# Performance work log

Measured on AMD Instinct MI355X. Metric: run time of the kernel, lower is better.

The kernel has to match this reference:

```python
import jax, jax.numpy as jnp
import numpy as np

N = 50000
E = 800000
F_IN = 2      # num_node_features
H = 2         # heads
C = 64        # embedding_size (per-head out channels)
HID = 128     # hidden_size (message dim)
B = 512       # number of messages
NEG_SLOPE = 0.2


def gatv2_conv(x, src, dst, edge_attr, Wl, bl, Wr, br, We, att, bias):
    # x: [N, F_IN]; src/dst: [E]; edge_attr: [E, 1]
    n = x.shape[0]
    xl = (x @ Wl + bl).reshape(n, H, C)   # source transform (lin_l)
    xr = (x @ Wr + br).reshape(n, H, C)   # target transform (lin_r)
    ea = (edge_attr @ We).reshape(-1, H, C)
    m = xl[src] + xr[dst] + ea                      # [E, H, C]
    e = jnp.where(m > 0, m, NEG_SLOPE * m)          # LeakyReLU
    score = jnp.einsum('ehc,hc->eh', e, att)        # [E, H]
    # scatter-softmax over incoming edges of each target node
    smax = jax.ops.segment_max(score, dst, num_segments=n)
    smax = jnp.where(jnp.isfinite(smax), smax, 0.0)
    ex = jnp.exp(score - smax[dst])
    denom = jax.ops.segment_sum(ex, dst, num_segments=n)
    alpha = ex / (denom[dst] + 1e-16)               # [E, H]
    out = jax.ops.segment_sum(xl[src] * alpha[:, :, None], dst, num_segments=n)
    return out.reshape(n, H * C) + bias


def setup_inputs() -> dict:
    key = jax.random.key(0)
    ks = jax.random.split(key, 20)
    s = 0.1
    inp = {
        'message': jax.random.normal(ks[0], (B, HID), jnp.float32),
        'x': jax.random.normal(ks[1], (N, F_IN), jnp.float32),
        'edge_index': jax.random.randint(ks[2], (2, E), 0, N, jnp.int32),
        'edge_attr': jax.random.normal(ks[3], (E, 1), jnp.float32),
    }
    def conv_params(base):
        return {
            'Wl': jax.random.normal(ks[base], (F_IN, H * C)) * s,
            'bl': jnp.zeros((H * C,), jnp.float32),
            'Wr': jax.random.normal(ks[base + 1], (F_IN, H * C)) * s,
            'br': jnp.zeros((H * C,), jnp.float32),
            'We': jax.random.normal(ks[base + 2], (1, H * C)) * s,
            'att': jax.random.normal(ks[base + 3], (H, C)) * s,
            'bias': jnp.zeros((H * C,), jnp.float32),
        }
    p1 = {k + '1': v for k, v in conv_params(4).items()}
    p2 = {k + '2': v for k, v in conv_params(8).items()}
    inp.update(p1)
    inp.update(p2)
    inp['Wfc'] = jax.random.normal(ks[12], (HID, H * C)) * s
    inp['bfc'] = jnp.zeros((H * C,), jnp.float32)
    return inp


def reference(message, x, edge_index, edge_attr,
              Wl1, bl1, Wr1, br1, We1, att1, bias1,
              Wl2, bl2, Wr2, br2, We2, att2, bias2,
              Wfc, bfc):
    src, dst = edge_index[0], edge_index[1]
    # conv1 output is computed but unused in the original forward (conv2 takes x again)
    h1 = jax.nn.relu(gatv2_conv(x, src, dst, edge_attr, Wl1, bl1, Wr1, br1, We1, att1, bias1))
    h = jax.nn.relu(gatv2_conv(x, src, dst, edge_attr, Wl2, bl2, Wr2, br2, We2, att2, bias2))
    msg = jnp.concatenate([message, message], axis=0)      # [2B, HID]
    msg_emb = msg @ Wfc + bfc                              # [2B, H*C]
    dot = h @ msg_emb.T                                    # [N, 2B]
    return jax.nn.softmax(dot, axis=0)
```

## Files before the change

kernel.cpp:

```cpp
#include <hip/hip_runtime.h>
#include <hip/hip_bf16.h>
#include <hip/hip_cooperative_groups.h>

namespace cg = cooperative_groups;

#define N_NODES 50000
#define N_PAD   50048
#define N_EDGES 800000
#define GRID    512
#define BLK     256
#define STRIDE  (GRID*BLK)
#define CHUNK   98
#define NTILES  782
#define NB_SCAN 196

typedef __attribute__((ext_vector_type(8))) short short8;
typedef __attribute__((ext_vector_type(16))) float f32x16;

struct Params {
  const float* msg; const float* x; const int* ei; const float* ea;
  const float* Wl; const float* bl; const float* Wr; const float* br;
  const float* We; const float* att; const float* bias;
  const float* Wfc; const float* bfc;
  float4* rec; float* nodeF;
  __hip_bfloat16* me_hi; __hip_bfloat16* me_lo;
  int* cnt; float* colsum; int* offs; int* cursor; int* bsum;
  float* dout;
};

template<int PASS>
__device__ __forceinline__ void mfma_tile(const Params& P, int tile, char* SMEM)
{
  short8* Bt = (short8*)SMEM;
  float* colacc = (float*)(SMEM + 32768);
  float* xp     = (float*)(SMEM + 32768);
  float* rcol   = (float*)(SMEM + 50176);

  const int tid = threadIdx.x;
  const int l = tid & 63, w = tid >> 6;
  const int rt = w >> 1, ct = w & 1;
  const int lrow = l & 31, lhalf = l >> 5;
  const int m0 = tile * 64;
  const int row = m0 + rt * 32 + lrow;

  float c0a = 0.f, c0b = 0.f, c0d = 0.f, c1a = 0.f, c1b = 0.f, c1d = 0.f;
  bool live = row < N_NODES;
  if (live) {
    const float* nf = P.nodeF + (size_t)row * 8;
    float D0 = nf[0], A00 = nf[1], A10 = nf[2];
    float D1 = nf[3], A01 = nf[4], A11 = nf[5];
    float r0 = 1.0f / (D0 + 1e-16f), r1 = 1.0f / (D1 + 1e-16f);
    c0a = A00 * r0; c0b = A10 * r0; c0d = D0 * r0;
    c1a = A01 * r1; c1b = A11 * r1; c1d = D1 * r1;
  }
  short8 a_hi[8], a_lo[8];
  #pragma unroll
  for (int ks = 0; ks < 8; ++ks) {
    int k0 = ks * 16 + lhalf * 8;
    float ca = (ks < 4) ? c0a : c1a;
    float cbv = (ks < 4) ? c0b : c1b;
    float cd = (ks < 4) ? c0d : c1d;
    float wA[8], wB[8], wC[8], wD[8];
    *(float4*)&wA[0] = *(const float4*)(P.Wl + k0);
    *(float4*)&wA[4] = *(const float4*)(P.Wl + k0 + 4);
    *(float4*)&wB[0] = *(const float4*)(P.Wl + 128 + k0);
    *(float4*)&wB[4] = *(const float4*)(P.Wl + 128 + k0 + 4);
    *(float4*)&wC[0] = *(const float4*)(P.bl + k0);
    *(float4*)&wC[4] = *(const float4*)(P.bl + k0 + 4);
    *(float4*)&wD[0] = *(const float4*)(P.bias + k0);
    *(float4*)&wD[4] = *(const float4*)(P.bias + k0 + 4);
    short8 hi8, lo8;
    #pragma unroll
    for (int j = 0; j < 8; ++j) {
      float v = ca * wA[j] + cbv * wB[j] + cd * wC[j] + wD[j];
      v = (live && v > 0.f) ? v : 0.f;
      __hip_bfloat16 hb = __float2bfloat16(v);
      float rem = v - __bfloat162float(hb);
      __hip_bfloat16 lb = __float2bfloat16(rem);
      short hs, ls;
      __builtin_memcpy(&hs, &hb, 2);
      __builtin_memcpy(&ls, &lb, 2);
      hi8[j] = hs; lo8[j] = ls;
    }
    a_hi[ks] = hi8; a_lo[ks] = lo8;
  }

  for (int cb = 0; cb < 8; ++cb) {
    __syncthreads();
    #pragma unroll
    for (int q = 0; q < 4; ++q) {
      int lin = q * 256 + tid;
      int col = lin >> 4, ku = lin & 15;
      int slot = col * 16 + (ku ^ (col & 7));
      size_t gb = ((size_t)(cb * 64 + col) << 7) + ku * 8;
      Bt[slot] = *(const short8*)(P.me_hi + gb);
      Bt[1024 + slot] = *(const short8*)(P.me_lo + gb);
    }
    __syncthreads();

    f32x16 acc = {0.f};
    #pragma unroll
    for (int ks = 0; ks < 8; ++ks) {
      int ku = ks * 2 + lhalf;
      int colB = ct * 32 + lrow;
      int slot = colB * 16 + (ku ^ (colB & 7));
      short8 bh = Bt[slot];
      short8 blo = Bt[1024 + slot];
      acc = __builtin_amdgcn_mfma_f32_32x32x16_bf16(a_hi[ks], bh, acc, 0, 0, 0);
      acc = __builtin_amdgcn_mfma_f32_32x32x16_bf16(a_lo[ks], bh, acc, 0, 0, 0);
      acc = __builtin_amdgcn_mfma_f32_32x32x16_bf16(a_hi[ks], blo, acc, 0, 0, 0);
    }

    if (PASS == 0) {
      float csum = 0.f;
      #pragma unroll
      for (int i = 0; i < 16; ++i) {
        int grow = m0 + rt * 32 + (i & 3) + 8 * (i >> 2) + 4 * lhalf;
        csum += (grow < N_NODES) ? __expf(acc[i]) : 0.f;
      }
      csum += __shfl_xor(csum, 32);
      if (l < 32) colacc[rt * 512 + cb * 64 + ct * 32 + l] += csum;
    } else {
      #pragma unroll
      for (int i = 0; i < 16; ++i) {
        int rl = rt * 32 + (i & 3) + 8 * (i >> 2) + 4 * lhalf;
        xp[rl * 68 + ct * 32 + lrow] = __expf(acc[i]);
      }
      __syncthreads();
      #pragma unroll
      for (int q = 0; q < 4; ++q) {
        int fid = q * 256 + tid;
        int rl = fid >> 4, c4 = fid & 15;
        int grow = m0 + rl;
        float4 v = *(float4*)&xp[rl * 68 + c4 * 4];
        float4 s = *(const float4*)&rcol[cb * 64 + c4 * 4];
        v.x *= s.x; v.y *= s.y; v.z *= s.z; v.w *= s.w;
        if (grow < N_NODES) {
          *(float4*)&P.dout[(size_t)grow * 1024 + cb * 64 + c4 * 4] = v;
          *(float4*)&P.dout[(size_t)grow * 1024 + 512 + cb * 64 + c4 * 4] = v;
        }
      }
    }
  }
}

__global__ __launch_bounds__(BLK, 2) void k_all(Params P)
{
  cg::grid_group gg = cg::this_grid();
  __shared__ __align__(16) char SMEM[52224];
  const int b = blockIdx.x, t = threadIdx.x;

  if (b < 256) {
    float* mrow = (float*)SMEM;
    int r = 2 * b + (t >> 7);
    int col = t & 127;
    mrow[t] = P.msg[r * 128 + col];
    __syncthreads();
    int base = (t >> 7) * 128;
    float acc = P.bfc[col];
    #pragma unroll 8
    for (int k = 0; k < 128; ++k) acc = fmaf(mrow[base + k], P.Wfc[k * 128 + col], acc);
    __hip_bfloat16 hi = __float2bfloat16(acc);
    P.me_hi[r * 128 + col] = hi;
    P.me_lo[r * 128 + col] = __float2bfloat16(acc - __bfloat162float(hi));
  } else if (b < 454) {
    int i = (b - 256) * 256 + t;
    if (i < N_NODES + 512) P.cnt[i] = 0;
  }
  gg.sync();

  for (int e = b * BLK + t; e < N_EDGES; e += STRIDE)
    atomicAdd(&P.cnt[P.ei[N_EDGES + e]], 1);
  gg.sync();

  {
    int* sh = (int*)SMEM;
    int base = b * CHUNK;
    if (t < 128) sh[t] = 0;
    __syncthreads();
    int v = 0;
    if (t < CHUNK && base + t < N_NODES) { v = P.cnt[base + t]; sh[t] = v; }
    __syncthreads();
    #pragma unroll
    for (int off = 1; off < 128; off <<= 1) {
      int u = (t < 128 && t >= off) ? sh[t - off] : 0;
      __syncthreads();
      if (t < 128) sh[t] += u;
      __syncthreads();
    }
    if (t < CHUNK && base + t < N_NODES) P.offs[base + t] = sh[t] - v;
    if (t == 0) P.bsum[b] = sh[127];
  }
  gg.sync();

  {
    int* eb = (int*)SMEM;
    int* s3 = eb + 512;
    int x0 = P.bsum[2 * t], x1 = P.bsum[2 * t + 1];
    s3[t] = x0 + x1;
    __syncthreads();
    #pragma unroll
    for (int off = 1; off < 256; off <<= 1) {
      int u = (t >= off) ? s3[t - off] : 0;
      __syncthreads();
      s3[t] += u;
      __syncthreads();
    }
    int p = t ? s3[t - 1] : 0;
    eb[2 * t] = p; eb[2 * t + 1] = p + x0;
    __syncthreads();
    int pb = eb[b];
    int base = b * CHUNK;
    if (t < CHUNK && base + t < N_NODES) {
      int o = P.offs[base + t] + pb;
      P.offs[base + t] = o;
      P.cursor[base + t] = o;
    }
    if (b == 0 && t == 0) P.offs[N_NODES] = N_EDGES;
  }
  gg.sync();

  for (int e = b * BLK + t; e < N_EDGES; e += STRIDE) {
    int s = P.ei[e], d = P.ei[N_EDGES + e];
    float x0s = P.x[2*s], x1s = P.x[2*s+1];
    float x0d = P.x[2*d], x1d = P.x[2*d+1];
    float av = P.ea[e];
    float s0 = 0.f, s1 = 0.f;
    #pragma unroll 8
    for (int k = 0; k < 64; ++k) {
      float m = P.bl[k] + P.br[k];
      m = fmaf(x0s, P.Wl[k], m);
      m = fmaf(x1s, P.Wl[128+k], m);
      m = fmaf(x0d, P.Wr[k], m);
      m = fmaf(x1d, P.Wr[128+k], m);
      m = fmaf(av, P.We[k], m);
      float lk = m > 0.f ? m : 0.2f * m;
      s0 = fmaf(lk, P.att[k], s0);
    }
    #pragma unroll 8
    for (int k = 64; k < 128; ++k) {
      float m = P.bl[k] + P.br[k];
      m = fmaf(x0s, P.Wl[k], m);
      m = fmaf(x1s, P.Wl[128+k], m);
      m = fmaf(x0d, P.Wr[k], m);
      m = fmaf(x1d, P.Wr[128+k], m);
      m = fmaf(av, P.We[k], m);
      float lk = m > 0.f ? m : 0.2f * m;
      s1 = fmaf(lk, P.att[k], s1);
    }
    int pos = atomicAdd(&P.cursor[d], 1);
    P.rec[pos] = make_float4(s0, s1, x0s, x1s);
  }
  gg.sync();

  {
    int n = b * BLK + t;
    if (n < N_NODES) {
      int a = P.offs[n], bb = P.offs[n + 1];
      float D0 = 0.f, A00 = 0.f, A10 = 0.f;
      float D1 = 0.f, A01 = 0.f, A11 = 0.f;
      for (int i = a; i < bb; ++i) {
        float4 r = P.rec[i];
        float e0 = __expf(r.x);
        float e1 = __expf(r.y);
        D0 += e0; A00 += e0 * r.z; A10 += e0 * r.w;
        D1 += e1; A01 += e1 * r.z; A11 += e1 * r.w;
      }
      float* nf = P.nodeF + (size_t)n * 8;
      nf[0] = D0; nf[1] = A00; nf[2] = A10;
      nf[3] = D1; nf[4] = A01; nf[5] = A11;
    }
  }
  gg.sync();

  {
    float* colacc = (float*)(SMEM + 32768);
    #pragma unroll
    for (int q = 0; q < 4; ++q) colacc[q * 256 + t] = 0.f;
    __syncthreads();
    for (int tile = b; tile < NTILES; tile += GRID)
      mfma_tile<0>(P, tile, SMEM);
    __syncthreads();
    atomicAdd(&P.colsum[t], colacc[t] + colacc[512 + t]);
    atomicAdd(&P.colsum[t + 256], colacc[256 + t] + colacc[768 + t]);
  }
  gg.sync();

  {
    float* rcol = (float*)(SMEM + 50176);
    rcol[t] = 1.0f / P.colsum[t];
    rcol[t + 256] = 1.0f / P.colsum[t + 256];
    __syncthreads();
    for (int tile = b; tile < NTILES; tile += GRID)
      mfma_tile<1>(P, tile, SMEM);
  }
}

__global__ __launch_bounds__(256) void k_zero(int* __restrict__ buf)
{
  int i = blockIdx.x * 256 + threadIdx.x;
  if (i < N_NODES + 512) buf[i] = 0;
}

__global__ __launch_bounds__(256) void k_hist(
    const int* __restrict__ ei, int* __restrict__ cnt)
{
  int e = blockIdx.x * 256 + threadIdx.x;
  if (e >= N_EDGES) return;
  atomicAdd(&cnt[ei[N_EDGES + e]], 1);
}

__global__ __launch_bounds__(256) void k_scan1(
    const int* __restrict__ cnt, int* __restrict__ offs, int* __restrict__ bsum)
{
  __shared__ int sh[256];
  int b = blockIdx.x, t = threadIdx.x;
  int i = b * 256 + t;
  int v = (i < N_NODES) ? cnt[i] : 0;
  sh[t] = v;
  __syncthreads();
  #pragma unroll
  for (int off = 1; off < 256; off <<= 1) {
    int u = (t >= off) ? sh[t - off] : 0;
    __syncthreads();
    sh[t] += u;
    __syncthreads();
  }
  if (i < N_NODES) offs[i] = sh[t] - v;
  if (t == 255) bsum[b] = sh[255];
}

__global__ __launch_bounds__(256) void k_scan2(int* __restrict__ bsum)
{
  __shared__ int sh[256];
  int t = threadIdx.x;
  int v = (t < NB_SCAN) ? bsum[t] : 0;
  sh[t] = v;
  __syncthreads();
  #pragma unroll
  for (int off = 1; off < 256; off <<= 1) {
    int u = (t >= off) ? sh[t - off] : 0;
    __syncthreads();
    sh[t] += u;
    __syncthreads();
  }
  if (t < NB_SCAN) bsum[t] = sh[t] - v;
}

__global__ __launch_bounds__(256) void k_scan3(
    int* __restrict__ offs, const int* __restrict__ bsum, int* __restrict__ cursor)
{
  int b = blockIdx.x, t = threadIdx.x;
  int i = b * 256 + t;
  if (i < N_NODES) {
    int o = offs[i] + bsum[b];
    offs[i] = o;
    cursor[i] = o;
  }
  if (b == 0 && t == 0) offs[N_NODES] = N_EDGES;
}

__global__ __launch_bounds__(256) void k_scatter(Params P)
{
  int e = blockIdx.x * 256 + threadIdx.x;
  if (e >= N_EDGES) return;
  int s = P.ei[e], d = P.ei[N_EDGES + e];
  float x0s = P.x[2*s], x1s = P.x[2*s+1];
  float x0d = P.x[2*d], x1d = P.x[2*d+1];
  float av = P.ea[e];
  float s0 = 0.f, s1 = 0.f;
  #pragma unroll 8
  for (int k = 0; k < 64; ++k) {
    float m = P.bl[k] + P.br[k];
    m = fmaf(x0s, P.Wl[k], m);
    m = fmaf(x1s, P.Wl[128+k], m);
    m = fmaf(x0d, P.Wr[k], m);
    m = fmaf(x1d, P.Wr[128+k], m);
    m = fmaf(av, P.We[k], m);
    float lk = m > 0.f ? m : 0.2f * m;
    s0 = fmaf(lk, P.att[k], s0);
  }
  #pragma unroll 8
  for (int k = 64; k < 128; ++k) {
    float m = P.bl[k] + P.br[k];
    m = fmaf(x0s, P.Wl[k], m);
    m = fmaf(x1s, P.Wl[128+k], m);
    m = fmaf(x0d, P.Wr[k], m);
    m = fmaf(x1d, P.Wr[128+k], m);
    m = fmaf(av, P.We[k], m);
    float lk = m > 0.f ? m : 0.2f * m;
    s1 = fmaf(lk, P.att[k], s1);
  }
  int pos = atomicAdd(&P.cursor[d], 1);
  P.rec[pos] = make_float4(s0, s1, x0s, x1s);
}

__global__ __launch_bounds__(256) void k_gather(Params P)
{
  int n = blockIdx.x * 256 + threadIdx.x;
  if (n >= N_NODES) return;
  int a = P.offs[n], b = P.offs[n + 1];
  float D0 = 0.f, A00 = 0.f, A10 = 0.f;
  float D1 = 0.f, A01 = 0.f, A11 = 0.f;
  for (int i = a; i < b; ++i) {
    float4 r = P.rec[i];
    float e0 = __expf(r.x);
    float e1 = __expf(r.y);
    D0 += e0; A00 += e0 * r.z; A10 += e0 * r.w;
    D1 += e1; A01 += e1 * r.z; A11 += e1 * r.w;
  }
  float* nf = P.nodeF + (size_t)n * 8;
  nf[0] = D0; nf[1] = A00; nf[2] = A10;
  nf[3] = D1; nf[4] = A01; nf[5] = A11;
}

__global__ __launch_bounds__(128) void k_fc(Params P)
{
  int j = blockIdx.x, k = threadIdx.x;
  __shared__ float mrow[128];
  mrow[k] = P.msg[j*128 + k];
  __syncthreads();
  float acc = P.bfc[k];
  #pragma unroll 8
  for (int t = 0; t < 128; ++t) acc = fmaf(mrow[t], P.Wfc[t*128 + k], acc);
  __hip_bfloat16 hi = __float2bfloat16(acc);
  P.me_hi[j*128 + k] = hi;
  P.me_lo[j*128 + k] = __float2bfloat16(acc - __bfloat162float(hi));
}

template<int PASS>
__global__ __launch_bounds__(256, 2) void k_mfma(Params P)
{
  __shared__ __align__(16) char SMEM[52224];
  int tid = threadIdx.x;
  if (PASS == 0) {
    float* colacc = (float*)(SMEM + 32768);
    #pragma unroll
    for (int q = 0; q < 4; ++q) colacc[q * 256 + tid] = 0.f;
    __syncthreads();
    mfma_tile<0>(P, blockIdx.x, SMEM);
    __syncthreads();
    atomicAdd(&P.colsum[tid], colacc[tid] + colacc[512 + tid]);
    atomicAdd(&P.colsum[tid + 256], colacc[256 + tid] + colacc[768 + tid]);
  } else {
    float* rcol = (float*)(SMEM + 50176);
    rcol[tid] = 1.0f / P.colsum[tid];
    rcol[tid + 256] = 1.0f / P.colsum[tid + 256];
    __syncthreads();
    mfma_tile<1>(P, blockIdx.x, SMEM);
  }
}

extern "C" void kernel_launch(void* const* d_in, const int* in_sizes, int n_in,
                              void* d_out, int out_size, void* d_ws, size_t ws_size,
                              hipStream_t stream)
{
  Params P;
  P.msg = (const float*)d_in[0];
  P.x   = (const float*)d_in[1];
  P.ei  = (const int*)d_in[2];
  P.ea  = (const float*)d_in[3];
  P.Wl   = (const float*)d_in[11];
  P.bl   = (const float*)d_in[12];
  P.Wr   = (const float*)d_in[13];
  P.br   = (const float*)d_in[14];
  P.We   = (const float*)d_in[15];
  P.att  = (const float*)d_in[16];
  P.bias = (const float*)d_in[17];
  P.Wfc  = (const float*)d_in[18];
  P.bfc  = (const float*)d_in[19];

  char* p = (char*)d_ws;
  P.rec = (float4*)p;                    p += (size_t)N_EDGES * 16;
  P.nodeF = (float*)p;                   p += (size_t)N_NODES * 8 * 4;
  P.me_hi = (__hip_bfloat16*)p;          p += 512 * 128 * 2;
  P.me_lo = (__hip_bfloat16*)p;          p += 512 * 128 * 2;
  P.cnt = (int*)p;                       p += (size_t)N_NODES * 4;
  P.colsum = (float*)p;                  p += 512 * 4;
  P.offs = (int*)p;                      p += (size_t)(N_NODES + 1) * 4;
  P.cursor = (int*)p;                    p += (size_t)N_NODES * 4;
  P.bsum = (int*)p;                      p += GRID * 4;
  P.dout = (float*)d_out;

  int maxBlk = 0;
  hipError_t qerr = hipOccupancyMaxActiveBlocksPerMultiprocessor(&maxBlk, k_all, BLK, 0);
  if (qerr == hipSuccess && maxBlk >= 2) {
    void* args[] = { &P };
    hipError_t lerr = hipLaunchCooperativeKernel((void*)k_all, dim3(GRID), dim3(BLK),
                                                 args, 0, stream);
    if (lerr == hipSuccess) return;
  }

  k_zero<<<(N_NODES + 512 + 255) / 256, 256, 0, stream>>>(P.cnt);
  k_hist<<<(N_EDGES + 255) / 256, 256, 0, stream>>>(P.ei, P.cnt);
  k_scan1<<<NB_SCAN, 256, 0, stream>>>(P.cnt, P.offs, P.bsum);
  k_scan2<<<1, 256, 0, stream>>>(P.bsum);
  k_scan3<<<NB_SCAN, 256, 0, stream>>>(P.offs, P.bsum, P.cursor);
  k_scatter<<<(N_EDGES + 255) / 256, 256, 0, stream>>>(P);
  k_gather<<<(N_NODES + 255) / 256, 256, 0, stream>>>(P);
  k_fc<<<512, 128, 0, stream>>>(P);
  k_mfma<0><<<NTILES, 256, 0, stream>>>(P);
  k_mfma<1><<<NTILES, 256, 0, stream>>>(P);
}
```

Baseline: 216.0 us.

## Drop LDS staging in MFMA tiles, raise cooperative grid to 3 blocks/CU, pack edge weights

The MFMA tile stage now loads B fragments straight from global memory instead of staging them through a swizzled LDS buffer. Column sums are accumulated with LDS atomics, and the normalize pass writes scalar outputs directly, with no LDS transpose. Shrinking LDS lets the cooperative kernel run 768 blocks at 3 per CU, so the scan chunking is adjusted to match. Edge-score weights are packed once into an interleaved float4 array so the per-edge loop issues fewer loads. The trade-off is uncoalesced scalar output stores and repeated global/L2 reads of B, in exchange for higher occupancy and fewer barriers.

```diff
diff --git a/kernel.cpp b/kernel.cpp
--- a/kernel.cpp
+++ b/kernel.cpp
@@ -7,10 +7,10 @@
 #define N_NODES 50000
 #define N_PAD   50048
 #define N_EDGES 800000
-#define GRID    512
+#define GRID    768
 #define BLK     256
 #define STRIDE  (GRID*BLK)
-#define CHUNK   98
+#define CHUNK   66
 #define NTILES  782
 #define NB_SCAN 196
 
@@ -25,17 +25,13 @@
   float4* rec; float* nodeF;
   __hip_bfloat16* me_hi; __hip_bfloat16* me_lo;
   int* cnt; float* colsum; int* offs; int* cursor; int* bsum;
+  float* w6;
   float* dout;
 };
 
 template<int PASS>
-__device__ __forceinline__ void mfma_tile(const Params& P, int tile, char* SMEM)
-{
-  short8* Bt = (short8*)SMEM;
-  float* colacc = (float*)(SMEM + 32768);
-  float* xp     = (float*)(SMEM + 32768);
-  float* rcol   = (float*)(SMEM + 50176);
-
+__device__ __forceinline__ void mfma_tile(const Params& P, int tile, float* colacc)
+{
   const int tid = threadIdx.x;
   const int l = tid & 63, w = tid >> 6;
   const int rt = w >> 1, ct = w & 1;
@@ -85,27 +81,17 @@
     a_hi[ks] = hi8; a_lo[ks] = lo8;
   }
 
+  const size_t bbase = (size_t)(ct * 32 + lrow) * 128 + lhalf * 8;
+
   for (int cb = 0; cb < 8; ++cb) {
-    __syncthreads();
-    #pragma unroll
-    for (int q = 0; q < 4; ++q) {
-      int lin = q * 256 + tid;
-      int col = lin >> 4, ku = lin & 15;
-      int slot = col * 16 + (ku ^ (col & 7));
-      size_t gb = ((size_t)(cb * 64 + col) << 7) + ku * 8;
-      Bt[slot] = *(const short8*)(P.me_hi + gb);
-      Bt[1024 + slot] = *(const short8*)(P.me_lo + gb);
-    }
-    __syncthreads();
+    const __hip_bfloat16* ph = P.me_hi + bbase + (size_t)cb * 8192;
+    const __hip_bfloat16* pl = P.me_lo + bbase + (size_t)cb * 8192;
 
     f32x16 acc = {0.f};
     #pragma unroll
     for (int ks = 0; ks < 8; ++ks) {
-      int ku = ks * 2 + lhalf;
-      int colB = ct * 32 + lrow;
-      int slot = colB * 16 + (ku ^ (colB & 7));
-      short8 bh = Bt[slot];
-      short8 blo = Bt[1024 + slot];
+      short8 bh = *(const short8*)(ph + ks * 16);
+      short8 blo = *(const short8*)(pl + ks * 16);
       acc = __builtin_amdgcn_mfma_f32_32x32x16_bf16(a_hi[ks], bh, acc, 0, 0, 0);
       acc = __builtin_amdgcn_mfma_f32_32x32x16_bf16(a_lo[ks], bh, acc, 0, 0, 0);
       acc = __builtin_amdgcn_mfma_f32_32x32x16_bf16(a_hi[ks], blo, acc, 0, 0, 0);
@@ -119,35 +105,28 @@
         csum += (grow < N_NODES) ? __expf(acc[i]) : 0.f;
       }
       csum += __shfl_xor(csum, 32);
-      if (l < 32) colacc[rt * 512 + cb * 64 + ct * 32 + l] += csum;
+      if (l < 32)
+        atomicAdd(&colacc[cb * 64 + ct * 32 + l], csum);
     } else {
+      int col = cb * 64 + ct * 32 + lrow;
+      float rS = 1.0f / P.colsum[col];
       #pragma unroll
       for (int i = 0; i < 16; ++i) {
-        int rl = rt * 32 + (i & 3) + 8 * (i >> 2) + 4 * lhalf;
-        xp[rl * 68 + ct * 32 + lrow] = __expf(acc[i]);
-      }
-      __syncthreads();
-      #pragma unroll
-      for (int q = 0; q < 4; ++q) {
-        int fid = q * 256 + tid;
-        int rl = fid >> 4, c4 = fid & 15;
-        int grow = m0 + rl;
-        float4 v = *(float4*)&xp[rl * 68 + c4 * 4];
-        float4 s = *(const float4*)&rcol[cb * 64 + c4 * 4];
-        v.x *= s.x; v.y *= s.y; v.z *= s.z; v.w *= s.w;
+        int grow = m0 + rt * 32 + (i & 3) + 8 * (i >> 2) + 4 * lhalf;
         if (grow < N_NODES) {
-          *(float4*)&P.dout[(size_t)grow * 1024 + cb * 64 + c4 * 4] = v;
-          *(float4*)&P.dout[(size_t)grow * 1024 + 512 + cb * 64 + c4 * 4] = v;
+          float o = __expf(acc[i]) * rS;
+          P.dout[(size_t)grow * 1024 + col] = o;
+          P.dout[(size_t)grow * 1024 + 512 + col] = o;
         }
       }
     }
   }
 }
 
-__global__ __launch_bounds__(BLK, 2) void k_all(Params P)
+__global__ __launch_bounds__(BLK, 3) void k_all(Params P)
 {
   cg::grid_group gg = cg::this_grid();
-  __shared__ __align__(16) char SMEM[52224];
+  __shared__ __align__(16) char SMEM[4096];
   const int b = blockIdx.x, t = threadIdx.x;
 
   if (b < 256) {
@@ -166,6 +145,12 @@
   } else if (b < 454) {
     int i = (b - 256) * 256 + t;
     if (i < N_NODES + 512) P.cnt[i] = 0;
+  } else if (b == 454 && t < 128) {
+    int k = t;
+    float4 a = make_float4(P.bl[k] + P.br[k], P.Wl[k], P.Wl[128 + k], P.Wr[k]);
+    float4 c = make_float4(P.Wr[128 + k], P.We[k], P.att[k], 0.f);
+    *(float4*)&P.w6[k * 8] = a;
+    *(float4*)&P.w6[k * 8 + 4] = c;
   }
   gg.sync();
 
@@ -195,9 +180,9 @@
 
   {
     int* eb = (int*)SMEM;
-    int* s3 = eb + 512;
-    int x0 = P.bsum[2 * t], x1 = P.bsum[2 * t + 1];
-    s3[t] = x0 + x1;
+    int* s3 = eb + 768;
+    int x0 = P.bsum[3 * t], x1 = P.bsum[3 * t + 1], x2 = P.bsum[3 * t + 2];
+    s3[t] = x0 + x1 + x2;
     __syncthreads();
     #pragma unroll
     for (int off = 1; off < 256; off <<= 1) {
@@ -207,7 +192,7 @@
       __syncthreads();
     }
     int p = t ? s3[t - 1] : 0;
-    eb[2 * t] = p; eb[2 * t + 1] = p + x0;
+    eb[3 * t] = p; eb[3 * t + 1] = p + x0; eb[3 * t + 2] = p + x0 + x1;
     __syncthreads();
     int pb = eb[b];
     int base = b * CHUNK;
@@ -220,36 +205,39 @@
   }
   gg.sync();
 
-  for (int e = b * BLK + t; e < N_EDGES; e += STRIDE) {
-    int s = P.ei[e], d = P.ei[N_EDGES + e];
-    float x0s = P.x[2*s], x1s = P.x[2*s+1];
-    float x0d = P.x[2*d], x1d = P.x[2*d+1];
-    float av = P.ea[e];
-    float s0 = 0.f, s1 = 0.f;
-    #pragma unroll 8
-    for (int k = 0; k < 64; ++k) {
-      float m = P.bl[k] + P.br[k];
-      m = fmaf(x0s, P.Wl[k], m);
-      m = fmaf(x1s, P.Wl[128+k], m);
-      m = fmaf(x0d, P.Wr[k], m);
-      m = fmaf(x1d, P.Wr[128+k], m);
-      m = fmaf(av, P.We[k], m);
-      float lk = m > 0.f ? m : 0.2f * m;
-      s0 = fmaf(lk, P.att[k], s0);
-    }
-    #pragma unroll 8
-    for (int k = 64; k < 128; ++k) {
-      float m = P.bl[k] + P.br[k];
-      m = fmaf(x0s, P.Wl[k], m);
-      m = fmaf(x1s, P.Wl[128+k], m);
-      m = fmaf(x0d, P.Wr[k], m);
-      m = fmaf(x1d, P.Wr[128+k], m);
-      m = fmaf(av, P.We[k], m);
-      float lk = m > 0.f ? m : 0.2f * m;
-      s1 = fmaf(lk, P.att[k], s1);
-    }
-    int pos = atomicAdd(&P.cursor[d], 1);
-    P.rec[pos] = make_float4(s0, s1, x0s, x1s);
+  {
+    const float4* W4 = (const float4*)P.w6;
+    for (int e = b * BLK + t; e < N_EDGES; e += STRIDE) {
+      int s = P.ei[e], d = P.ei[N_EDGES + e];
+      float x0s = P.x[2*s], x1s = P.x[2*s+1];
+      float x0d = P.x[2*d], x1d = P.x[2*d+1];
+      float av = P.ea[e];
+      float s0 = 0.f, s1 = 0.f;
+      #pragma unroll 8
+      for (int k = 0; k < 64; ++k) {
+        float4 a = W4[2*k], c = W4[2*k+1];
+        float m = a.x;
+        m = fmaf(x0s, a.y, m);
+        m = fmaf(x1s, a.z, m);
+        m = fmaf(x0d, a.w, m);
+        m = fmaf(x1d, c.x, m);
+        m = fmaf(av,  c.y, m);
+        s0 = fmaf(fmaxf(m, 0.2f * m), c.z, s0);
+      }
+      #pragma unroll 8
+      for (int k = 64; k < 128; ++k) {
+        float4 a = W4[2*k], c = W4[2*k+1];
+        float m = a.x;
+        m = fmaf(x0s, a.y, m);
+        m = fmaf(x1s, a.z, m);
+        m = fmaf(x0d, a.w, m);
+        m = fmaf(x1d, c.x, m);
+        m = fmaf(av,  c.y, m);
+        s1 = fmaf(fmaxf(m, 0.2f * m), c.z, s1);
+      }
+      int pos = atomicAdd(&P.cursor[d], 1);
+      P.rec[pos] = make_float4(s0, s1, x0s, x1s);
+    }
   }
   gg.sync();
 
@@ -274,26 +262,20 @@
   gg.sync();
 
   {
-    float* colacc = (float*)(SMEM + 32768);
+    float* colacc = (float*)SMEM;
     #pragma unroll
-    for (int q = 0; q < 4; ++q) colacc[q * 256 + t] = 0.f;
+    for (int q = 0; q < 2; ++q) colacc[q * 256 + t] = 0.f;
     __syncthreads();
     for (int tile = b; tile < NTILES; tile += GRID)
-      mfma_tile<0>(P, tile, SMEM);
-    __syncthreads();
-    atomicAdd(&P.colsum[t], colacc[t] + colacc[512 + t]);
-    atomicAdd(&P.colsum[t + 256], colacc[256 + t] + colacc[768 + t]);
-  }
-  gg.sync();
-
-  {
-    float* rcol = (float*)(SMEM + 50176);
-    rcol[t] = 1.0f / P.colsum[t];
-    rcol[t + 256] = 1.0f / P.colsum[t + 256];
-    __syncthreads();
-    for (int tile = b; tile < NTILES; tile += GRID)
-      mfma_tile<1>(P, tile, SMEM);
-  }
+      mfma_tile<0>(P, tile, colacc);
+    __syncthreads();
+    atomicAdd(&P.colsum[t], colacc[t]);
+    atomicAdd(&P.colsum[t + 256], colacc[t + 256]);
+  }
+  gg.sync();
+
+  for (int tile = b; tile < NTILES; tile += GRID)
+    mfma_tile<1>(P, tile, nullptr);
 }
 
 __global__ __launch_bounds__(256) void k_zero(int* __restrict__ buf)
@@ -360,10 +342,22 @@
   if (b == 0 && t == 0) offs[N_NODES] = N_EDGES;
 }
 
+__global__ void k_w6(Params P)
+{
+  int k = threadIdx.x;
+  if (k < 128) {
+    float4 a = make_float4(P.bl[k] + P.br[k], P.Wl[k], P.Wl[128 + k], P.Wr[k]);
+    float4 c = make_float4(P.Wr[128 + k], P.We[k], P.att[k], 0.f);
+    *(float4*)&P.w6[k * 8] = a;
+    *(float4*)&P.w6[k * 8 + 4] = c;
+  }
+}
+
 __global__ __launch_bounds__(256) void k_scatter(Params P)
 {
   int e = blockIdx.x * 256 + threadIdx.x;
   if (e >= N_EDGES) return;
+  const float4* W4 = (const float4*)P.w6;
   int s = P.ei[e], d = P.ei[N_EDGES + e];
   float x0s = P.x[2*s], x1s = P.x[2*s+1];
   float x0d = P.x[2*d], x1d = P.x[2*d+1];
@@ -371,25 +365,25 @@
   float s0 = 0.f, s1 = 0.f;
   #pragma unroll 8
   for (int k = 0; k < 64; ++k) {
-    float m = P.bl[k] + P.br[k];
-    m = fmaf(x0s, P.Wl[k], m);
-    m = fmaf(x1s, P.Wl[128+k], m);
-    m = fmaf(x0d, P.Wr[k], m);
-    m = fmaf(x1d, P.Wr[128+k], m);
-    m = fmaf(av, P.We[k], m);
-    float lk = m > 0.f ? m : 0.2f * m;
-    s0 = fmaf(lk, P.att[k], s0);
+    float4 a = W4[2*k], c = W4[2*k+1];
+    float m = a.x;
+    m = fmaf(x0s, a.y, m);
+    m = fmaf(x1s, a.z, m);
+    m = fmaf(x0d, a.w, m);
+    m = fmaf(x1d, c.x, m);
+    m = fmaf(av,  c.y, m);
+    s0 = fmaf(fmaxf(m, 0.2f * m), c.z, s0);
   }
   #pragma unroll 8
   for (int k = 64; k < 128; ++k) {
-    float m = P.bl[k] + P.br[k];
-    m = fmaf(x0s, P.Wl[k], m);
-    m = fmaf(x1s, P.Wl[128+k], m);
-    m = fmaf(x0d, P.Wr[k], m);
-    m = fmaf(x1d, P.Wr[128+k], m);
-    m = fmaf(av, P.We[k], m);
-    float lk = m > 0.f ? m : 0.2f * m;
-    s1 = fmaf(lk, P.att[k], s1);
+    float4 a = W4[2*k], c = W4[2*k+1];
+    float m = a.x;
+    m = fmaf(x0s, a.y, m);
+    m = fmaf(x1s, a.z, m);
+    m = fmaf(x0d, a.w, m);
+    m = fmaf(x1d, c.x, m);
+    m = fmaf(av,  c.y, m);
+    s1 = fmaf(fmaxf(m, 0.2f * m), c.z, s1);
   }
   int pos = atomicAdd(&P.cursor[d], 1);
   P.rec[pos] = make_float4(s0, s1, x0s, x1s);
@@ -429,25 +423,19 @@
 }
 
 template<int PASS>
-__global__ __launch_bounds__(256, 2) void k_mfma(Params P)
-{
-  __shared__ __align__(16) char SMEM[52224];
+__global__ __launch_bounds__(256, 3) void k_mfma(Params P)
+{
+  __shared__ __align__(16) float colacc[512];
   int tid = threadIdx.x;
   if (PASS == 0) {
-    float* colacc = (float*)(SMEM + 32768);
-    #pragma unroll
-    for (int q = 0; q < 4; ++q) colacc[q * 256 + tid] = 0.f;
-    __syncthreads();
-    mfma_tile<0>(P, blockIdx.x, SMEM);
-    __syncthreads();
-    atomicAdd(&P.colsum[tid], colacc[tid] + colacc[512 + tid]);
-    atomicAdd(&P.colsum[tid + 256], colacc[256 + tid] + colacc[768 + tid]);
+    colacc[tid] = 0.f; colacc[tid + 256] = 0.f;
+    __syncthreads();
+    mfma_tile<0>(P, blockIdx.x, colacc);
+    __syncthreads();
+    atomicAdd(&P.colsum[tid], colacc[tid]);
+    atomicAdd(&P.colsum[tid + 256], colacc[tid + 256]);
   } else {
-    float* rcol = (float*)(SMEM + 50176);
-    rcol[tid] = 1.0f / P.colsum[tid];
-    rcol[tid + 256] = 1.0f / P.colsum[tid + 256];
-    __syncthreads();
-    mfma_tile<1>(P, blockIdx.x, SMEM);
+    mfma_tile<1>(P, blockIdx.x, nullptr);
   }
 }
 
@@ -480,11 +468,12 @@
   P.offs = (int*)p;                      p += (size_t)(N_NODES + 1) * 4;
   P.cursor = (int*)p;                    p += (size_t)N_NODES * 4;
   P.bsum = (int*)p;                      p += GRID * 4;
+  P.w6 = (float*)p;                      p += 128 * 8 * 4;
   P.dout = (float*)d_out;
 
   int maxBlk = 0;
   hipError_t qerr = hipOccupancyMaxActiveBlocksPerMultiprocessor(&maxBlk, k_all, BLK, 0);
-  if (qerr == hipSuccess && maxBlk >= 2) {
+  if (qerr == hipSuccess && maxBlk >= 3) {
     void* args[] = { &P };
     hipError_t lerr = hipLaunchCooperativeKernel((void*)k_all, dim3(GRID), dim3(BLK),
                                                  args, 0, stream);
@@ -496,6 +485,7 @@
   k_scan1<<<NB_SCAN, 256, 0, stream>>>(P.cnt, P.offs, P.bsum);
   k_scan2<<<1, 256, 0, stream>>>(P.bsum);
   k_scan3<<<NB_SCAN, 256, 0, stream>>>(P.offs, P.bsum, P.cursor);
+  k_w6<<<1, 128, 0, stream>>>(P);
   k_scatter<<<(N_EDGES + 255) / 256, 256, 0, stream>>>(P);
   k_gather<<<(N_NODES + 255) / 256, 256, 0, stream>>>(P);
   k_fc<<<512, 128, 0, stream>>>(P);
```

After: 290.8 us. 1.35x slower.
